# Kernel tuning notes

Hardware: AMD Instinct MI355X
Metric: run time of the kernel (lower is better)

The kernel has to match this reference:

```python
import jax, jax.numpy as jnp
import numpy as np


def fwht(x):
    """Fast Walsh-Hadamard transform over last axis (power-of-2 length), normalized by 1/sqrt(n).
    Matches matmul_hadU with K=1 (pure Hadamard rotation)."""
    orig_shape = x.shape
    n = orig_shape[-1]
    x = x.reshape(-1, n)
    h = 1
    while h < n:
        x = x.reshape(-1, n // (2 * h), 2, h)
        a = x[:, :, 0, :]
        b = x[:, :, 1, :]
        x = jnp.stack([a + b, a - b], axis=2)
        h *= 2
    x = x.reshape(orig_shape)
    return x * (1.0 / np.sqrt(n)).astype(np.float32)


def setup_inputs() -> dict:
    key = jax.random.key(0)
    k1, k2, k3, k4, k5 = jax.random.split(key, 5)
    B, S, n, m = 2, 2048, 4096, 4096
    CODEBOOK = 65536  # 2^16 E8P codes, each decoding an 8-dim lattice point
    inp = jax.random.normal(k1, (B, S, n), dtype=jnp.float32)
    # SU/SV are random sign-like diagonal rescales in QuIP; use unit-variance floats here
    SU = jax.random.normal(k2, (n,), dtype=jnp.float32)
    SV = jax.random.normal(k3, (m,), dtype=jnp.float32)
    grid = jax.random.normal(k4, (CODEBOOK, 8), dtype=jnp.float32) * 0.1
    Qidxs = jax.random.randint(k5, (m, n // 8), 0, CODEBOOK, dtype=jnp.int32)
    return {"input": inp, "SU": SU, "SV": SV, "grid": grid, "Qidxs": Qidxs}


def reference(input, SU, SV, grid, Qidxs):
    n = SU.shape[0]
    m = SV.shape[0]
    x = input.reshape(-1, n) * SU          # diagonal rescale by SU
    x = fwht(x)                             # left Hadamard rotation
    # Dequantize packed E8P codebook: each 16-bit code -> 8 weights
    W = grid[Qidxs].reshape(m, n)           # [m, n]
    x = x @ W.T                             # dense GEMM against dequantized weight
    x = fwht(x)                             # right Hadamard rotation
    x = x * SV                              # diagonal rescale by SV
    return x.reshape(input.shape[:-1] + (m,))
```

## Files before the change

kernel.cpp:

```cpp
#include <hip/hip_runtime.h>
#include <stdint.h>

typedef __bf16 bf16x8 __attribute__((ext_vector_type(8)));
typedef float f32x4 __attribute__((ext_vector_type(4)));

__device__ __forceinline__ unsigned int f2bf(float f) {
  unsigned int u = __float_as_uint(f);
  return (u + 0x7fffu + ((u >> 16) & 1u)) >> 16;
}
__device__ __forceinline__ unsigned int pack2(float a, float b) {
  return f2bf(a) | (f2bf(b) << 16);
}

__device__ __forceinline__ void fwht16(float v[16]) {
#pragma unroll
  for (int s = 0; s < 4; ++s) {
    const int h = 1 << s;
#pragma unroll
    for (int i = 0; i < 16; ++i) {
      if (!(i & h)) {
        float a = v[i], b = v[i ^ h];
        v[i] = a + b;
        v[i ^ h] = a - b;
      }
    }
  }
}

#define LP(i) ((i) + ((i) >> 5))

__global__ void __launch_bounds__(256) k_prep(const float* __restrict__ X,
                                              const float* __restrict__ SU,
                                              unsigned short* __restrict__ Xh,
                                              const int* __restrict__ Qidxs,
                                              const float* __restrict__ G,
                                              unsigned short* __restrict__ Wh) {
  __shared__ float lds[4224];
  const int t = threadIdx.x;
  if (blockIdx.x >= 4096) {
    int e = (blockIdx.x - 4096) * 256 + t;
    int idx = Qidxs[e];
    const float4* g = (const float4*)(G + (size_t)idx * 8);
    float4 a = g[0], b = g[1];
    uint4 o;
    o.x = pack2(a.x, a.y);
    o.y = pack2(a.z, a.w);
    o.z = pack2(b.x, b.y);
    o.w = pack2(b.z, b.w);
    ((uint4*)Wh)[e] = o;
    return;
  }
  const size_t row = blockIdx.x;
  const float4* xr = (const float4*)(X + row * 4096);
  const float4* su = (const float4*)SU;
  float v[16];
#pragma unroll
  for (int q = 0; q < 4; ++q) {
    float4 a = xr[4 * t + q], s = su[4 * t + q];
    v[4 * q + 0] = a.x * s.x;
    v[4 * q + 1] = a.y * s.y;
    v[4 * q + 2] = a.z * s.z;
    v[4 * q + 3] = a.w * s.w;
  }
  fwht16(v);
#pragma unroll
  for (int q = 0; q < 4; ++q) {
    int i0 = 16 * t + 4 * q;
    *(float4*)&lds[LP(i0)] = make_float4(v[4 * q], v[4 * q + 1], v[4 * q + 2], v[4 * q + 3]);
  }
  __syncthreads();
  const int b = ((t >> 4) << 8) | (t & 15);
#pragma unroll
  for (int j = 0; j < 16; ++j) { int i = b + 16 * j; v[j] = lds[LP(i)]; }
  fwht16(v);
#pragma unroll
  for (int j = 0; j < 16; ++j) { int i = b + 16 * j; lds[LP(i)] = v[j]; }
  __syncthreads();
#pragma unroll
  for (int j = 0; j < 16; ++j) { int i = t + 256 * j; v[j] = lds[LP(i)]; }
  fwht16(v);
  unsigned short* orow = Xh + row * 4096;
#pragma unroll
  for (int j = 0; j < 16; ++j)
    orow[t + 256 * j] = (unsigned short)f2bf(v[j] * 0.015625f);
}

__device__ __forceinline__ void gl2lds16(const unsigned short* g, unsigned short* l) {
  __builtin_amdgcn_global_load_lds(
      (const __attribute__((address_space(1))) void*)g,
      (__attribute__((address_space(3))) void*)l, 16, 0, 0);
}

#define BARX() __builtin_amdgcn_s_barrier()
#define WAITV4() asm volatile("s_waitcnt vmcnt(4)" ::: "memory")

#define RD_A(dst, mm)                                                          \
  _Pragma("unroll") for (int kh = 0; kh < 2; ++kh)                             \
      dst[kh] = *(const bf16x8*)&sAp[(((wr) << 7) + ((mm) << 4) + frow) * 64 + \
                                     ((((kh << 2) + jb) ^ sw) << 3)];
#define RD_B()                                                                 \
  _Pragma("unroll") for (int n = 0; n < 4; ++n)                                \
      _Pragma("unroll") for (int kh = 0; kh < 2; ++kh)                         \
          bq[n][kh] = *(const bf16x8*)&sBp[(((wc) << 6) + (n << 4) + frow) * 64 + \
                                           ((((kh << 2) + jb) ^ sw) << 3)];
#define MF(mm, buf)                                                            \
  _Pragma("unroll") for (int n = 0; n < 4; ++n)                                \
      _Pragma("unroll") for (int kh = 0; kh < 2; ++kh)                         \
          acc[(mm)][n] = __builtin_amdgcn_mfma_f32_16x16x32_bf16(              \
              buf[kh], bq[n][kh], acc[(mm)][n], 0, 0, 0);

__global__ void __launch_bounds__(512, 2)
k_gemm_bt(const unsigned short* __restrict__ A,
          const unsigned short* __restrict__ B,
          float* __restrict__ C) {
  const int K = 4096, N = 4096;
  __shared__ unsigned short sA[2][256 * 64];
  __shared__ unsigned short sB[2][256 * 64];
  const int tid = threadIdx.x;
  const int lane = tid & 63;
  const int wave = tid >> 6;
  const int wr = wave >> 2;
  const int wc = wave & 3;
  const int frow = lane & 15;
  const int jb = lane >> 4;
  const int sw = frow & 7;
  const int bn = blockIdx.x, bm = blockIdx.y;
  const size_t rowA0 = (size_t)bm * 256;
  const size_t rowB0 = (size_t)bn * 256;

  f32x4 acc[8][4] = {};

  auto stage = [&](const unsigned short* __restrict__ G, size_t row0,
                   unsigned short* dst, int h, int ktile) {
    const int kt = (ktile < 64 ? ktile : 0) << 6;
#pragma unroll
    for (int l = 0; l < 2; ++l) {
      const int c = (l << 9) + tid;
      const int r = c >> 3;
      const int jg = (c & 7) ^ (r & 7);
      gl2lds16(G + (row0 + (size_t)((h << 7) + r)) * K + kt + (jg << 3),
               dst + (h << 13) + (c << 3));
    }
  };

  auto group = [&](int p, int gA, int gB) {
    const unsigned short* sAp = sA[p];
    const unsigned short* sBp = sB[p];
    unsigned short* sAn = (unsigned short*)sA[p ^ 1];
    unsigned short* sBn = (unsigned short*)sB[p];
    bf16x8 bq[4][2];
    bf16x8 r0[2], r1[2], r2[2];
    RD_A(r0, 0);
    RD_B();
    RD_A(r1, 1);
    RD_A(r2, 2);
    stage(A, rowA0, sAn, 0, gA);
    BARX();
    __builtin_amdgcn_s_setprio(1);
    MF(0, r0);
    RD_A(r0, 3);
    MF(1, r1);
    __builtin_amdgcn_s_setprio(0);
    BARX();
    RD_A(r1, 4);
    stage(A, rowA0, sAn, 1, gA);
    BARX();
    __builtin_amdgcn_s_setprio(1);
    MF(2, r2);
    RD_A(r2, 5);
    MF(3, r0);
    __builtin_amdgcn_s_setprio(0);
    BARX();
    RD_A(r0, 6);
    stage(B, rowB0, sBn, 0, gB);
    BARX();
    __builtin_amdgcn_s_setprio(1);
    MF(4, r1);
    RD_A(r1, 7);
    MF(5, r2);
    __builtin_amdgcn_s_setprio(0);
    BARX();
    stage(B, rowB0, sBn, 1, gB);
    BARX();
    __builtin_amdgcn_s_setprio(1);
    MF(6, r0);
    MF(7, r1);
    __builtin_amdgcn_s_setprio(0);
    WAITV4();
    BARX();
  };

  stage(B, rowB0, sB[0], 0, 0);
  stage(B, rowB0, sB[0], 1, 0);
  stage(A, rowA0, sA[0], 0, 0);
  stage(A, rowA0, sA[0], 1, 0);
  stage(B, rowB0, sB[1], 0, 1);
  stage(B, rowB0, sB[1], 1, 1);
  WAITV4();
  BARX();

#pragma unroll 1
  for (int i = 0; i < 32; ++i) {
    group(0, 2 * i + 1, 2 * i + 2);
    group(1, 2 * i + 2, 2 * i + 3);
  }

  const int rbase = bm * 256 + (wr << 7) + (jb << 2);
  const int cbase = bn * 256 + (wc << 6) + frow;
#pragma unroll
  for (int m = 0; m < 8; ++m)
#pragma unroll
    for (int n = 0; n < 4; ++n) {
      float* cp = C + (size_t)(rbase + (m << 4)) * N + cbase + (n << 4);
#pragma unroll
      for (int r = 0; r < 4; ++r) cp[(size_t)r * N] = acc[m][n][r];
    }
}

__global__ void __launch_bounds__(256) k_fwht_out(float* __restrict__ Y,
                                                  const float* __restrict__ SV) {
  __shared__ float lds[4224];
  const int t = threadIdx.x;
  const size_t row = blockIdx.x;
  float* yrow = Y + row * 4096;
  const float4* yr = (const float4*)yrow;
  float v[16];
#pragma unroll
  for (int q = 0; q < 4; ++q) {
    float4 a = yr[4 * t + q];
    v[4 * q + 0] = a.x;
    v[4 * q + 1] = a.y;
    v[4 * q + 2] = a.z;
    v[4 * q + 3] = a.w;
  }
  fwht16(v);
#pragma unroll
  for (int q = 0; q < 4; ++q) {
    int i0 = 16 * t + 4 * q;
    *(float4*)&lds[LP(i0)] = make_float4(v[4 * q], v[4 * q + 1], v[4 * q + 2], v[4 * q + 3]);
  }
  __syncthreads();
  const int b = ((t >> 4) << 8) | (t & 15);
#pragma unroll
  for (int j = 0; j < 16; ++j) { int i = b + 16 * j; v[j] = lds[LP(i)]; }
  fwht16(v);
#pragma unroll
  for (int j = 0; j < 16; ++j) { int i = b + 16 * j; lds[LP(i)] = v[j]; }
  __syncthreads();
#pragma unroll
  for (int j = 0; j < 16; ++j) { int i = t + 256 * j; v[j] = lds[LP(i)]; }
  fwht16(v);
#pragma unroll
  for (int j = 0; j < 16; ++j) {
    int i = t + 256 * j;
    yrow[i] = v[j] * SV[i] * 0.015625f;
  }
}

extern "C" void kernel_launch(void* const* d_in, const int* in_sizes, int n_in,
                              void* d_out, int out_size, void* d_ws, size_t ws_size,
                              hipStream_t stream) {
  const float* X     = (const float*)d_in[0];
  const float* SU    = (const float*)d_in[1];
  const float* SV    = (const float*)d_in[2];
  const float* G     = (const float*)d_in[3];
  const int*   Qidxs = (const int*)d_in[4];
  float* out = (float*)d_out;

  unsigned short* Xh = (unsigned short*)d_ws;
  unsigned short* Wh = Xh + (size_t)4096 * 4096;

  k_prep<<<4096 + 8192, 256, 0, stream>>>(X, SU, Xh, Qidxs, G, Wh);
  k_gemm_bt<<<dim3(16, 16), 512, 0, stream>>>(Xh, Wh, out);
  k_fwht_out<<<4096, 256, 0, stream>>>(out, SV);
}
```

Measured before the change: 271.1 us.

## Restructure GEMM main loop into K-half quadrant phases with cross-tile fragment prefetch

Replaces the per-tile group schedule, which iterated over 8 M-fragments each needing both K halves, with four quadrant phases of 16 MFMAs each (4 M-fragments by 4 N-fragments, one K half). The first A and B fragments of the next tile are prefetched from LDS into registers before the last phase, with an earlier vmcnt(2) wait. The aim is better overlap of LDS reads, global-to-LDS staging and MFMA work, and fewer barrier-delimited phases per tile. In exchange it holds more fragment registers live and depends on tight vmcnt ordering, which could cost occupancy or correctness.

```diff
diff --git a/kernel.cpp b/kernel.cpp
--- a/kernel.cpp
+++ b/kernel.cpp
@@ -93,21 +93,23 @@
 
 #define BARX() __builtin_amdgcn_s_barrier()
 #define WAITV4() asm volatile("s_waitcnt vmcnt(4)" ::: "memory")
-
-#define RD_A(dst, mm)                                                          \
-  _Pragma("unroll") for (int kh = 0; kh < 2; ++kh)                             \
-      dst[kh] = *(const bf16x8*)&sAp[(((wr) << 7) + ((mm) << 4) + frow) * 64 + \
-                                     ((((kh << 2) + jb) ^ sw) << 3)];
-#define RD_B()                                                                 \
+#define WAITV2() asm volatile("s_waitcnt vmcnt(2)" ::: "memory")
+
+#define RD_A4(dst, buf, mb, kh)                                                \
+  _Pragma("unroll") for (int m = 0; m < 4; ++m)                                \
+      dst[m] = *(const bf16x8*)&buf[(((wr) << 7) + (((mb) + m) << 4) + frow) * 64 + \
+                                    (((((kh) << 2) + jb) ^ sw) << 3)];
+#define RD_B4(dst, buf, kh)                                                    \
   _Pragma("unroll") for (int n = 0; n < 4; ++n)                                \
-      _Pragma("unroll") for (int kh = 0; kh < 2; ++kh)                         \
-          bq[n][kh] = *(const bf16x8*)&sBp[(((wc) << 6) + (n << 4) + frow) * 64 + \
-                                           ((((kh << 2) + jb) ^ sw) << 3)];
-#define MF(mm, buf)                                                            \
-  _Pragma("unroll") for (int n = 0; n < 4; ++n)                                \
-      _Pragma("unroll") for (int kh = 0; kh < 2; ++kh)                         \
-          acc[(mm)][n] = __builtin_amdgcn_mfma_f32_16x16x32_bf16(              \
-              buf[kh], bq[n][kh], acc[(mm)][n], 0, 0, 0);
+      dst[n] = *(const bf16x8*)&buf[(((wc) << 6) + (n << 4) + frow) * 64 +     \
+                                    (((((kh) << 2) + jb) ^ sw) << 3)];
+#define MFC(mb, As, Bs)                                                        \
+  __builtin_amdgcn_s_setprio(1);                                               \
+  _Pragma("unroll") for (int m = 0; m < 4; ++m)                                \
+      _Pragma("unroll") for (int n = 0; n < 4; ++n)                            \
+          acc[(mb) + m][n] = __builtin_amdgcn_mfma_f32_16x16x32_bf16(          \
+              As[m], Bs[n], acc[(mb) + m][n], 0, 0, 0);                        \
+  __builtin_amdgcn_s_setprio(0);
 
 __global__ void __launch_bounds__(512, 2)
 k_gemm_bt(const unsigned short* __restrict__ A,
@@ -129,6 +131,7 @@
   const size_t rowB0 = (size_t)bn * 256;
 
   f32x4 acc[8][4] = {};
+  bf16x8 c0A[4], bK0[4];
 
   auto stage = [&](const unsigned short* __restrict__ G, size_t row0,
                    unsigned short* dst, int h, int ktile) {
@@ -143,53 +146,6 @@
     }
   };
 
-  auto group = [&](int p, int gA, int gB) {
-    const unsigned short* sAp = sA[p];
-    const unsigned short* sBp = sB[p];
-    unsigned short* sAn = (unsigned short*)sA[p ^ 1];
-    unsigned short* sBn = (unsigned short*)sB[p];
-    bf16x8 bq[4][2];
-    bf16x8 r0[2], r1[2], r2[2];
-    RD_A(r0, 0);
-    RD_B();
-    RD_A(r1, 1);
-    RD_A(r2, 2);
-    stage(A, rowA0, sAn, 0, gA);
-    BARX();
-    __builtin_amdgcn_s_setprio(1);
-    MF(0, r0);
-    RD_A(r0, 3);
-    MF(1, r1);
-    __builtin_amdgcn_s_setprio(0);
-    BARX();
-    RD_A(r1, 4);
-    stage(A, rowA0, sAn, 1, gA);
-    BARX();
-    __builtin_amdgcn_s_setprio(1);
-    MF(2, r2);
-    RD_A(r2, 5);
-    MF(3, r0);
-    __builtin_amdgcn_s_setprio(0);
-    BARX();
-    RD_A(r0, 6);
-    stage(B, rowB0, sBn, 0, gB);
-    BARX();
-    __builtin_amdgcn_s_setprio(1);
-    MF(4, r1);
-    RD_A(r1, 7);
-    MF(5, r2);
-    __builtin_amdgcn_s_setprio(0);
-    BARX();
-    stage(B, rowB0, sBn, 1, gB);
-    BARX();
-    __builtin_amdgcn_s_setprio(1);
-    MF(6, r0);
-    MF(7, r1);
-    __builtin_amdgcn_s_setprio(0);
-    WAITV4();
-    BARX();
-  };
-
   stage(B, rowB0, sB[0], 0, 0);
   stage(B, rowB0, sB[0], 1, 0);
   stage(A, rowA0, sA[0], 0, 0);
@@ -198,11 +154,42 @@
   stage(B, rowB0, sB[1], 1, 1);
   WAITV4();
   BARX();
+  RD_A4(c0A, sA[0], 0, 0);
+  RD_B4(bK0, sB[0], 0);
 
 #pragma unroll 1
-  for (int i = 0; i < 32; ++i) {
-    group(0, 2 * i + 1, 2 * i + 2);
-    group(1, 2 * i + 2, 2 * i + 3);
+  for (int g = 0; g < 64; ++g) {
+    const int p = g & 1;
+    const unsigned short* sAp = sA[p];
+    const unsigned short* sBp = sB[p];
+    const unsigned short* sApN = sA[p ^ 1];
+    const unsigned short* sBpN = sB[p ^ 1];
+    unsigned short* sAn = (unsigned short*)sA[p ^ 1];
+    unsigned short* sBn = (unsigned short*)sB[p];
+    bf16x8 c1A[4], c2A[4], c3A[4], bK1[4];
+    RD_A4(c1A, sAp, 4, 0);
+    RD_B4(bK1, sBp, 1);
+    stage(A, rowA0, sAn, 0, g + 1);
+    BARX();
+    MFC(0, c0A, bK0);
+    BARX();
+    RD_A4(c2A, sAp, 0, 1);
+    stage(A, rowA0, sAn, 1, g + 1);
+    BARX();
+    MFC(4, c1A, bK0);
+    BARX();
+    RD_A4(c3A, sAp, 4, 1);
+    stage(B, rowB0, sBn, 0, g + 2);
+    BARX();
+    MFC(0, c2A, bK1);
+    WAITV2();
+    BARX();
+    RD_A4(c0A, sApN, 0, 0);
+    RD_B4(bK0, sBpN, 0);
+    stage(B, rowB0, sBn, 1, g + 2);
+    BARX();
+    MFC(4, c3A, bK1);
+    BARX();
   }
 
   const int rbase = bm * 256 + (wr << 7) + (jb << 2);
```

Result: slower. 289.0 us (+6.6%).
